# Kernel optimization log

Hardware: AMD Instinct MI355X
Metric: run time of the kernel (lower is better)

The kernel has to match this reference:

```python
import jax, jax.numpy as jnp
import numpy as np

WS = 8                    # window side
N = WS * WS               # tokens per window = 64
H_RES, W_RES = 64, 64     # input_resolution
HEADS = 16
DIM = 1024
HD = DIM // HEADS
SCALE = HD ** -0.5
TAB = 2 * WS - 1          # bias table length = 15
BATCH = 8
NW = (H_RES // WS) * (W_RES // WS)  # 64 windows per image
B_TOT = BATCH * NW        # 512


def _rel_coords():
    ch, cw = np.meshgrid(np.arange(WS), np.arange(WS), indexing='ij')
    coords = np.stack([ch.ravel(), cw.ravel()])           # (2, N)
    rel = coords[:, :, None] - coords[:, None, :]          # (2, N, N)
    return rel[0].astype(np.int32), rel[1].astype(np.int32)

_RADIUS, _AZIMUTH = _rel_coords()  # each (N, N), values in [-(WS-1), WS-1]


def setup_inputs() -> dict:
    key = jax.random.key(0)
    ks = jax.random.split(key, 10)
    return {
        'x': jax.random.normal(ks[0], (B_TOT, N, DIM), jnp.float32),
        'theta_max': jax.random.uniform(ks[1], (BATCH,), jnp.float32) * np.float32(np.pi),
        'qkv_w': jax.random.normal(ks[2], (3 * DIM, DIM), jnp.float32) * 0.02,
        'qkv_b': jax.random.normal(ks[3], (3 * DIM,), jnp.float32) * 0.02,
        'proj_w': jax.random.normal(ks[4], (DIM, DIM), jnp.float32) * 0.02,
        'proj_b': jax.random.normal(ks[5], (DIM,), jnp.float32) * 0.02,
        'a_p': jax.random.normal(ks[6], (TAB, HEADS), jnp.float32) * 0.02,
        'b_p': jax.random.normal(ks[7], (TAB, HEADS), jnp.float32) * 0.02,
        'a_r': jax.random.normal(ks[8], (TAB, HEADS), jnp.float32) * 0.02,
        'b_r': jax.random.normal(ks[9], (TAB, HEADS), jnp.float32) * 0.02,
    }


def reference(x, theta_max, qkv_w, qkv_b, proj_w, proj_b, a_p, b_p, a_r, b_r):
    B_, Nn, C = x.shape
    radius = jnp.asarray(_RADIUS)      # (N, N) signed ints
    azimuth = jnp.asarray(_AZIMUTH)    # (N, N) signed ints

    # qkv projection -> q, k, v of shape (B_, heads, N, head_dim)
    qkv = (x @ qkv_w.T + qkv_b).reshape(B_, Nn, 3, HEADS, HD).transpose(2, 0, 3, 1, 4)
    q, k, v = qkv[0] * SCALE, qkv[1], qkv[2]
    attn = jnp.einsum('bhid,bhjd->bhij', q, k)  # (B_, h, N, N)

    # A_phi: azimuth bias (torch negative indexing == mod TAB)
    az_idx = azimuth % TAB
    az_ang = azimuth.astype(jnp.float32) * jnp.float32(2.0 * np.pi / W_RES)
    A_phi = a_p[az_idx] * jnp.cos(az_ang)[..., None] + b_p[az_idx] * jnp.sin(az_ang)[..., None]  # (N, N, h)
    A_phi = A_phi.transpose(2, 0, 1)  # (h, N, N)

    # A_theta: radius bias scaled by per-image theta_max
    r_idx = radius % TAB
    nW = B_ // theta_max.shape[0]
    tmax = jnp.repeat(theta_max, nW).reshape(B_, 1, 1, 1)
    rn = radius.astype(jnp.float32)[None, :, :, None] * tmax / jnp.float32(H_RES)  # (B_, N, N, 1)
    A_theta = a_r[r_idx][None] * jnp.cos(rn) + b_r[r_idx][None] * jnp.sin(rn)      # (B_, N, N, h)
    A_theta = A_theta.transpose(0, 3, 1, 2)  # (B_, h, N, N)

    attn = jax.nn.softmax(attn + A_phi[None] + A_theta, axis=-1)
    out = jnp.einsum('bhij,bhjd->bhid', attn, v)             # (B_, h, N, hd)
    out = out.transpose(0, 2, 1, 3).reshape(B_, Nn, C)
    return out @ proj_w.T + proj_b
```

## Files before the change

kernel.cpp:

```cpp
#include <hip/hip_runtime.h>
#include <hip/hip_bf16.h>

#define DIMC   1024
#define HEADS  16
#define HDIM   64
#define NTOK   64
#define BTOT   512
#define TABL   15

typedef __attribute__((ext_vector_type(8))) short short8;
typedef __attribute__((ext_vector_type(4))) float f32x4;
typedef __attribute__((ext_vector_type(8))) unsigned short u16x8;

static __device__ __forceinline__ void gload_lds16(const void* g, void* l) {
    __builtin_amdgcn_global_load_lds((const __attribute__((address_space(1))) void*)g,
                                     (__attribute__((address_space(3))) void*)l, 16, 0, 0);
}

static __device__ __forceinline__ unsigned short f2bf(float f) {
    __hip_bfloat16 h = __float2bfloat16(f);
    return *(unsigned short*)&h;
}

__global__ void cvt_kernel(const float* __restrict__ in, unsigned short* __restrict__ out, int n4) {
    int stride = gridDim.x * blockDim.x;
    for (int i = blockIdx.x * blockDim.x + threadIdx.x; i < n4; i += stride) {
        float4 v = ((const float4*)in)[i];
        ushort4 o;
        o.x = f2bf(v.x); o.y = f2bf(v.y); o.z = f2bf(v.z); o.w = f2bf(v.w);
        ((ushort4*)out)[i] = o;
    }
}

template<int NMAT, int MODE>
__global__ __launch_bounds__(256, 2)
void gemm_bt(const unsigned short* __restrict__ A,
             const unsigned short* __restrict__ B,
             const float* __restrict__ bias,
             float* __restrict__ Cf, unsigned short* __restrict__ Cb)
{
    constexpr int K  = 1024;
    constexpr int BK = 32;
    __shared__ unsigned short Al[128 * BK];
    __shared__ unsigned short Bl[128 * BK];

    const int nbn  = NMAT / 128;
    const int bm   = blockIdx.x / nbn;
    const int bn   = blockIdx.x % nbn;
    const int tid  = threadIdx.x;
    const int lane = tid & 63;
    const int w    = tid >> 6;
    const int wm   = w >> 1, wn = w & 1;
    const int l15  = lane & 15, lg = lane >> 4;

    f32x4 acc[4][4] = {};

    const int rsub = lane >> 2;
    const int kcol = (lane & 3) * 8;
    const unsigned short* gA = A + (size_t)(bm * 128) * K;
    const unsigned short* gB = B + (size_t)(bn * 128) * K;

    for (int kt = 0; kt < K / BK; ++kt) {
        const int k0 = kt * BK;
        #pragma unroll
        for (int s = 0; s < 2; ++s) {
            int seg = w * 2 + s;
            int row = seg * 16 + rsub;
            gload_lds16(gA + (size_t)row * K + k0 + kcol, (char*)Al + seg * 1024);
            gload_lds16(gB + (size_t)row * K + k0 + kcol, (char*)Bl + seg * 1024);
        }
        __syncthreads();
        short8 af[4], bfr[4];
        #pragma unroll
        for (int mt = 0; mt < 4; ++mt)
            af[mt] = *(const short8*)&Al[(wm * 64 + mt * 16 + l15) * BK + lg * 8];
        #pragma unroll
        for (int nt = 0; nt < 4; ++nt)
            bfr[nt] = *(const short8*)&Bl[(wn * 64 + nt * 16 + l15) * BK + lg * 8];
        #pragma unroll
        for (int mt = 0; mt < 4; ++mt)
            #pragma unroll
            for (int nt = 0; nt < 4; ++nt)
                acc[mt][nt] = __builtin_amdgcn_mfma_f32_16x16x32_bf16(af[mt], bfr[nt], acc[mt][nt], 0, 0, 0);
        __syncthreads();
    }

    #pragma unroll
    for (int mt = 0; mt < 4; ++mt) {
        #pragma unroll
        for (int nt = 0; nt < 4; ++nt) {
            const int f = bn * 128 + wn * 64 + nt * 16 + l15;
            const float bv = bias[f];
            #pragma unroll
            for (int r = 0; r < 4; ++r) {
                const int m = bm * 128 + wm * 64 + mt * 16 + lg * 4 + r;
                float val = acc[mt][nt][r] + bv;
                if (MODE == 0) {
                    if (f < 1024) val *= 0.125f;
                    Cb[(size_t)m * NMAT + f] = f2bf(val);
                } else {
                    Cf[(size_t)m * NMAT + f] = val;
                }
            }
        }
    }
}

__global__ __launch_bounds__(256, 2)
void attn_kernel(const unsigned short* __restrict__ qkv,
                 const float* __restrict__ theta_max,
                 const float* __restrict__ a_p, const float* __restrict__ b_p,
                 const float* __restrict__ a_r, const float* __restrict__ b_r,
                 unsigned short* __restrict__ o_ws)
{
    const int bh = blockIdx.x;
    const int b  = bh >> 4;
    const int h  = bh & 15;
    const int tid = threadIdx.x, lane = tid & 63, w = tid >> 6;
    const int l15 = lane & 15, lg = lane >> 4;

    __shared__ unsigned short ql[64 * 64];
    __shared__ unsigned short kl[64 * 64];
    __shared__ unsigned short vtl[64 * 64];
    __shared__ float S[64 * 64];
    __shared__ unsigned short P[64 * 64];
    __shared__ float phiTab[15], thetaTab[15];

    if (tid < 15) {
        int az = tid - 7;
        int azm = az < 0 ? az + 15 : az;
        float ang = (float)az * 0.09817477042468103f;
        phiTab[tid] = a_p[azm * 16 + h] * cosf(ang) + b_p[azm * 16 + h] * sinf(ang);
    } else if (tid >= 32 && tid < 47) {
        int rr = tid - 39;
        int rm = rr < 0 ? rr + 15 : rr;
        float rn = (float)rr * theta_max[b >> 6] * 0.015625f;
        thetaTab[tid - 32] = a_r[rm * 16 + h] * cosf(rn) + b_r[rm * 16 + h] * sinf(rn);
    }

    const unsigned short* qg = qkv + (size_t)b * 64 * 3072 + h * 64;
    const unsigned short* kg = qg + 1024;
    const unsigned short* vg = qg + 2048;
    #pragma unroll
    for (int rep = 0; rep < 2; ++rep) {
        int idx = tid + rep * 256;
        int row = idx >> 3, seg = idx & 7;
        *(float4*)&ql[row * 64 + seg * 8] = *(const float4*)&qg[(size_t)row * 3072 + seg * 8];
        *(float4*)&kl[row * 64 + seg * 8] = *(const float4*)&kg[(size_t)row * 3072 + seg * 8];
        u16x8 vv = *(const u16x8*)&vg[(size_t)row * 3072 + seg * 8];
        #pragma unroll
        for (int e = 0; e < 8; ++e)
            vtl[(seg * 8 + e) * 64 + row] = vv[e];
    }
    __syncthreads();

    short8 aq[2];
    #pragma unroll
    for (int kc = 0; kc < 2; ++kc)
        aq[kc] = *(const short8*)&ql[(w * 16 + l15) * 64 + kc * 32 + lg * 8];
    f32x4 sacc[4] = {};
    #pragma unroll
    for (int nt = 0; nt < 4; ++nt)
        #pragma unroll
        for (int kc = 0; kc < 2; ++kc) {
            short8 bk = *(const short8*)&kl[(nt * 16 + l15) * 64 + kc * 32 + lg * 8];
            sacc[nt] = __builtin_amdgcn_mfma_f32_16x16x32_bf16(aq[kc], bk, sacc[nt], 0, 0, 0);
        }

    #pragma unroll
    for (int nt = 0; nt < 4; ++nt)
        #pragma unroll
        for (int r = 0; r < 4; ++r) {
            int i = w * 16 + lg * 4 + r;
            int j = nt * 16 + l15;
            int az = (i & 7) - (j & 7);
            int rr = (i >> 3) - (j >> 3);
            S[i * 64 + j] = sacc[nt][r] + phiTab[az + 7] + thetaTab[rr + 7];
        }
    __syncthreads();

    {
        int row = tid >> 2, q4 = tid & 3;
        float x[16];
        #pragma unroll
        for (int t = 0; t < 4; ++t) {
            float4 v = *(const float4*)&S[row * 64 + q4 * 16 + t * 4];
            x[t * 4 + 0] = v.x; x[t * 4 + 1] = v.y; x[t * 4 + 2] = v.z; x[t * 4 + 3] = v.w;
        }
        float mx = x[0];
        #pragma unroll
        for (int t = 1; t < 16; ++t) mx = fmaxf(mx, x[t]);
        mx = fmaxf(mx, __shfl_xor(mx, 1));
        mx = fmaxf(mx, __shfl_xor(mx, 2));
        float sum = 0.f;
        #pragma unroll
        for (int t = 0; t < 16; ++t) { x[t] = expf(x[t] - mx); sum += x[t]; }
        sum += __shfl_xor(sum, 1);
        sum += __shfl_xor(sum, 2);
        float inv = 1.0f / sum;
        #pragma unroll
        for (int t = 0; t < 16; ++t)
            P[row * 64 + q4 * 16 + t] = f2bf(x[t] * inv);
    }
    __syncthreads();

    short8 ap[2];
    #pragma unroll
    for (int kc = 0; kc < 2; ++kc)
        ap[kc] = *(const short8*)&P[(w * 16 + l15) * 64 + kc * 32 + lg * 8];
    f32x4 oacc[4] = {};
    #pragma unroll
    for (int dt = 0; dt < 4; ++dt)
        #pragma unroll
        for (int kc = 0; kc < 2; ++kc) {
            short8 bv = *(const short8*)&vtl[(dt * 16 + l15) * 64 + kc * 32 + lg * 8];
            oacc[dt] = __builtin_amdgcn_mfma_f32_16x16x32_bf16(ap[kc], bv, oacc[dt], 0, 0, 0);
        }
    #pragma unroll
    for (int dt = 0; dt < 4; ++dt)
        #pragma unroll
        for (int r = 0; r < 4; ++r) {
            int i = w * 16 + lg * 4 + r;
            int d = dt * 16 + l15;
            o_ws[(size_t)(b * 64 + i) * 1024 + h * 64 + d] = f2bf(oacc[dt][r]);
        }
}

extern "C" void kernel_launch(void* const* d_in, const int* in_sizes, int n_in,
                              void* d_out, int out_size, void* d_ws, size_t ws_size,
                              hipStream_t stream) {
    const float* x      = (const float*)d_in[0];
    const float* theta  = (const float*)d_in[1];
    const float* qkv_w  = (const float*)d_in[2];
    const float* qkv_b  = (const float*)d_in[3];
    const float* proj_w = (const float*)d_in[4];
    const float* proj_b = (const float*)d_in[5];
    const float* a_p    = (const float*)d_in[6];
    const float* b_p    = (const float*)d_in[7];
    const float* a_r    = (const float*)d_in[8];
    const float* b_r    = (const float*)d_in[9];
    float* out = (float*)d_out;

    char* ws = (char*)d_ws;
    unsigned short* xb    = (unsigned short*)(ws);
    unsigned short* wqkv  = (unsigned short*)(ws + 67108864);
    unsigned short* wproj = (unsigned short*)(ws + 73400320);
    unsigned short* qkvb  = (unsigned short*)(ws + 75497472);
    unsigned short* ob    = (unsigned short*)(ws + 276824064);

    cvt_kernel<<<2048, 256, 0, stream>>>(x,      xb,    33554432 / 4);
    cvt_kernel<<<1024, 256, 0, stream>>>(qkv_w,  wqkv,  3145728 / 4);
    cvt_kernel<<<512,  256, 0, stream>>>(proj_w, wproj, 1048576 / 4);

    gemm_bt<3072, 0><<<dim3(256 * 24), dim3(256), 0, stream>>>(xb, wqkv, qkv_b, nullptr, qkvb);

    attn_kernel<<<dim3(512 * 16), dim3(256), 0, stream>>>(qkvb, theta, a_p, b_p, a_r, b_r, ob);

    gemm_bt<1024, 1><<<dim3(256 * 8), dim3(256), 0, stream>>>(ob, wproj, proj_b, out, nullptr);
}
```

Before: 655.9 us.

## Keep attention softmax in registers, swizzle LDS tiles, re-layout GEMM LDS

The attention kernel now computes S transposed (K as the A operand), so each lane holds one query row's scores. It applies the bias, softmax and bf16 packing in registers and rebuilds the P operand with cross-lane shuffles, which removes the S and P LDS round trips and two barriers. Q/K/V tiles in LDS get XOR swizzles to avoid bank conflicts, and the GEMM LDS layout is changed to k-plane-major. It also switches expf to the faster __expf, at some accuracy risk and with complex shuffle-index logic.

```diff
diff --git a/kernel.cpp b/kernel.cpp
--- a/kernel.cpp
+++ b/kernel.cpp
@@ -40,9 +40,8 @@
              float* __restrict__ Cf, unsigned short* __restrict__ Cb)
 {
     constexpr int K  = 1024;
-    constexpr int BK = 32;
-    __shared__ unsigned short Al[128 * BK];
-    __shared__ unsigned short Bl[128 * BK];
+    __shared__ unsigned short Al[4096];
+    __shared__ unsigned short Bl[4096];
 
     const int nbn  = NMAT / 128;
     const int bm   = blockIdx.x / nbn;
@@ -55,28 +54,29 @@
 
     f32x4 acc[4][4] = {};
 
-    const int rsub = lane >> 2;
-    const int kcol = (lane & 3) * 8;
     const unsigned short* gA = A + (size_t)(bm * 128) * K;
     const unsigned short* gB = B + (size_t)(bn * 128) * K;
 
-    for (int kt = 0; kt < K / BK; ++kt) {
-        const int k0 = kt * BK;
+    for (int kt = 0; kt < K / 32; ++kt) {
+        const int k0 = kt * 32;
         #pragma unroll
         for (int s = 0; s < 2; ++s) {
-            int seg = w * 2 + s;
-            int row = seg * 16 + rsub;
-            gload_lds16(gA + (size_t)row * K + k0 + kcol, (char*)Al + seg * 1024);
-            gload_lds16(gB + (size_t)row * K + k0 + kcol, (char*)Bl + seg * 1024);
+            const int chunk = w * 2 + s;
+            const int plane = chunk >> 1;
+            const int r0    = (chunk & 1) * 64;
+            gload_lds16(gA + (size_t)(r0 + lane) * K + k0 + plane * 8,
+                        (char*)Al + plane * 2048 + r0 * 16);
+            gload_lds16(gB + (size_t)(r0 + lane) * K + k0 + plane * 8,
+                        (char*)Bl + plane * 2048 + r0 * 16);
         }
         __syncthreads();
         short8 af[4], bfr[4];
         #pragma unroll
         for (int mt = 0; mt < 4; ++mt)
-            af[mt] = *(const short8*)&Al[(wm * 64 + mt * 16 + l15) * BK + lg * 8];
+            af[mt] = *(const short8*)&Al[lg * 1024 + (wm * 64 + mt * 16 + l15) * 8];
         #pragma unroll
         for (int nt = 0; nt < 4; ++nt)
-            bfr[nt] = *(const short8*)&Bl[(wn * 64 + nt * 16 + l15) * BK + lg * 8];
+            bfr[nt] = *(const short8*)&Bl[lg * 1024 + (wn * 64 + nt * 16 + l15) * 8];
         #pragma unroll
         for (int mt = 0; mt < 4; ++mt)
             #pragma unroll
@@ -119,11 +119,9 @@
     const int tid = threadIdx.x, lane = tid & 63, w = tid >> 6;
     const int l15 = lane & 15, lg = lane >> 4;
 
-    __shared__ unsigned short ql[64 * 64];
-    __shared__ unsigned short kl[64 * 64];
-    __shared__ unsigned short vtl[64 * 64];
-    __shared__ float S[64 * 64];
-    __shared__ unsigned short P[64 * 64];
+    __shared__ unsigned short ql[4096];
+    __shared__ unsigned short kl[4096];
+    __shared__ unsigned short vtl[4096];
     __shared__ float phiTab[15], thetaTab[15];
 
     if (tid < 15) {
@@ -145,77 +143,96 @@
     for (int rep = 0; rep < 2; ++rep) {
         int idx = tid + rep * 256;
         int row = idx >> 3, seg = idx & 7;
-        *(float4*)&ql[row * 64 + seg * 8] = *(const float4*)&qg[(size_t)row * 3072 + seg * 8];
-        *(float4*)&kl[row * 64 + seg * 8] = *(const float4*)&kg[(size_t)row * 3072 + seg * 8];
+        int qslot = seg ^ (row & 7);
+        *(float4*)&ql[row * 64 + qslot * 8] = *(const float4*)&qg[(size_t)row * 3072 + seg * 8];
+        *(float4*)&kl[row * 64 + qslot * 8] = *(const float4*)&kg[(size_t)row * 3072 + seg * 8];
         u16x8 vv = *(const u16x8*)&vg[(size_t)row * 3072 + seg * 8];
         #pragma unroll
-        for (int e = 0; e < 8; ++e)
-            vtl[(seg * 8 + e) * 64 + row] = vv[e];
+        for (int e = 0; e < 8; ++e) {
+            int d = seg * 8 + e;
+            vtl[d * 64 + (row ^ ((e ^ seg) << 3))] = vv[e];
+        }
     }
     __syncthreads();
 
-    short8 aq[2];
+    const int qrow = w * 16 + l15;
+    short8 qf[2];
     #pragma unroll
     for (int kc = 0; kc < 2; ++kc)
-        aq[kc] = *(const short8*)&ql[(w * 16 + l15) * 64 + kc * 32 + lg * 8];
+        qf[kc] = *(const short8*)&ql[qrow * 64 + (((kc * 4 + lg) ^ (l15 & 7)) * 8)];
+
     f32x4 sacc[4] = {};
     #pragma unroll
-    for (int nt = 0; nt < 4; ++nt)
+    for (int jt = 0; jt < 4; ++jt) {
+        const int krow = jt * 16 + l15;
         #pragma unroll
         for (int kc = 0; kc < 2; ++kc) {
-            short8 bk = *(const short8*)&kl[(nt * 16 + l15) * 64 + kc * 32 + lg * 8];
-            sacc[nt] = __builtin_amdgcn_mfma_f32_16x16x32_bf16(aq[kc], bk, sacc[nt], 0, 0, 0);
-        }
-
-    #pragma unroll
-    for (int nt = 0; nt < 4; ++nt)
-        #pragma unroll
-        for (int r = 0; r < 4; ++r) {
-            int i = w * 16 + lg * 4 + r;
-            int j = nt * 16 + l15;
-            int az = (i & 7) - (j & 7);
-            int rr = (i >> 3) - (j >> 3);
-            S[i * 64 + j] = sacc[nt][r] + phiTab[az + 7] + thetaTab[rr + 7];
-        }
-    __syncthreads();
-
-    {
-        int row = tid >> 2, q4 = tid & 3;
-        float x[16];
+            short8 kf = *(const short8*)&kl[krow * 64 + (((kc * 4 + lg) ^ (l15 & 7)) * 8)];
+            sacc[jt] = __builtin_amdgcn_mfma_f32_16x16x32_bf16(kf, qf[kc], sacc[jt], 0, 0, 0);
+        }
+    }
+
+    float s[16];
+    const int i7 = l15 & 7;
+    const int ihi = w * 2 + (l15 >> 3);
+    float phiv[4];
+    #pragma unroll
+    for (int r = 0; r < 4; ++r)
+        phiv[r] = phiTab[i7 - ((lg * 4 + r) & 7) + 7];
+    #pragma unroll
+    for (int jt = 0; jt < 4; ++jt) {
+        float thv = thetaTab[ihi - jt * 2 - (lg >> 1) + 7];
+        #pragma unroll
+        for (int r = 0; r < 4; ++r)
+            s[jt * 4 + r] = sacc[jt][r] + phiv[r] + thv;
+    }
+
+    float mx = s[0];
+    #pragma unroll
+    for (int t = 1; t < 16; ++t) mx = fmaxf(mx, s[t]);
+    mx = fmaxf(mx, __shfl_xor(mx, 16));
+    mx = fmaxf(mx, __shfl_xor(mx, 32));
+    float sum = 0.f;
+    #pragma unroll
+    for (int t = 0; t < 16; ++t) { s[t] = __expf(s[t] - mx); sum += s[t]; }
+    sum += __shfl_xor(sum, 16);
+    sum += __shfl_xor(sum, 32);
+    const float inv = 1.0f / sum;
+
+    unsigned int W[4][2];
+    #pragma unroll
+    for (int jt = 0; jt < 4; ++jt)
+        #pragma unroll
+        for (int p = 0; p < 2; ++p)
+            W[jt][p] = (unsigned int)f2bf(s[jt * 4 + 2 * p] * inv)
+                     | ((unsigned int)f2bf(s[jt * 4 + 2 * p + 1] * inv) << 16);
+
+    const int srcA = l15 + (((lg << 1) & 3) << 4);
+    const int srcB = l15 + ((((lg << 1) + 1) & 3) << 4);
+    const bool hi = (lg >> 1) != 0;
+    union { unsigned int u[4]; short8 v; } ap[2];
+    #pragma unroll
+    for (int kc = 0; kc < 2; ++kc) {
         #pragma unroll
         for (int t = 0; t < 4; ++t) {
-            float4 v = *(const float4*)&S[row * 64 + q4 * 16 + t * 4];
-            x[t * 4 + 0] = v.x; x[t * 4 + 1] = v.y; x[t * 4 + 2] = v.z; x[t * 4 + 3] = v.w;
-        }
-        float mx = x[0];
-        #pragma unroll
-        for (int t = 1; t < 16; ++t) mx = fmaxf(mx, x[t]);
-        mx = fmaxf(mx, __shfl_xor(mx, 1));
-        mx = fmaxf(mx, __shfl_xor(mx, 2));
-        float sum = 0.f;
-        #pragma unroll
-        for (int t = 0; t < 16; ++t) { x[t] = expf(x[t] - mx); sum += x[t]; }
-        sum += __shfl_xor(sum, 1);
-        sum += __shfl_xor(sum, 2);
-        float inv = 1.0f / sum;
-        #pragma unroll
-        for (int t = 0; t < 16; ++t)
-            P[row * 64 + q4 * 16 + t] = f2bf(x[t] * inv);
-    }
-    __syncthreads();
-
-    short8 ap[2];
-    #pragma unroll
-    for (int kc = 0; kc < 2; ++kc)
-        ap[kc] = *(const short8*)&P[(w * 16 + l15) * 64 + kc * 32 + lg * 8];
+            int src = (t < 2) ? srcA : srcB;
+            unsigned int x0 = __shfl(W[kc * 2][t & 1], src);
+            unsigned int x1 = __shfl(W[kc * 2 + 1][t & 1], src);
+            ap[kc].u[t] = hi ? x1 : x0;
+        }
+    }
+
     f32x4 oacc[4] = {};
     #pragma unroll
-    for (int dt = 0; dt < 4; ++dt)
+    for (int dt = 0; dt < 4; ++dt) {
+        const int d = dt * 16 + l15;
+        const int sx = (d & 7) ^ (d >> 3);
         #pragma unroll
         for (int kc = 0; kc < 2; ++kc) {
-            short8 bv = *(const short8*)&vtl[(dt * 16 + l15) * 64 + kc * 32 + lg * 8];
-            oacc[dt] = __builtin_amdgcn_mfma_f32_16x16x32_bf16(ap[kc], bv, oacc[dt], 0, 0, 0);
-        }
+            short8 bv = *(const short8*)&vtl[d * 64 + (((kc * 4 + lg) ^ sx) * 8)];
+            oacc[dt] = __builtin_amdgcn_mfma_f32_16x16x32_bf16(ap[kc].v, bv, oacc[dt], 0, 0, 0);
+        }
+    }
     #pragma unroll
     for (int dt = 0; dt < 4; ++dt)
         #pragma unroll
```

Result: slower. 839.5 us (+28.0%).
